# Optimization experiments

Hardware: AMD Instinct MI355X
Metric: run time of the kernel (lower is better)

The kernel has to match this reference:

```python
import jax, jax.numpy as jnp
import numpy as np

B, N, D, H = 8, 2048, 128, 128  # batch, num_nodes, input_size, hidden_size


def setup_inputs() -> dict:
    key = jax.random.key(0)
    ks = jax.random.split(key, 10)
    s = 1.0 / np.sqrt(H)
    u = lambda k, shape: jax.random.uniform(k, shape, jnp.float32, -s, s)
    return {
        "x": jax.random.normal(ks[0], (B, N, D), jnp.float32),
        "adj_matrix": jax.random.randint(ks[1], (B, N, N), 0, 2, jnp.int32),
        # PyTorch LSTM params, gate order (i, f, g, o); forward + backward dirs
        "w_ih_f": u(ks[2], (4 * H, D)),
        "w_hh_f": u(ks[3], (4 * H, H)),
        "b_ih_f": u(ks[4], (4 * H,)),
        "b_hh_f": u(ks[5], (4 * H,)),
        "w_ih_b": u(ks[6], (4 * H, D)),
        "w_hh_b": u(ks[7], (4 * H, H)),
        "b_ih_b": u(ks[8], (4 * H,)),
        "b_hh_b": u(ks[9], (4 * H,)),
    }


def _lstm_last_h(xp, w_hh):
    # xp: [T, B, 4H] precomputed input projection + biases; returns final h [B, H]
    b = xp.shape[1]
    h0 = jnp.zeros((b, H), xp.dtype)
    c0 = jnp.zeros((b, H), xp.dtype)

    def step(carry, xt):
        h, c = carry
        gates = xt + h @ w_hh.T
        i, f, g, o = jnp.split(gates, 4, axis=-1)
        c = jax.nn.sigmoid(f) * c + jax.nn.sigmoid(i) * jnp.tanh(g)
        h = jax.nn.sigmoid(o) * jnp.tanh(c)
        return (h, c), None

    (hT, _), _ = jax.lax.scan(step, (h0, c0), xp)
    return hT


def reference(x, adj_matrix, w_ih_f, w_hh_f, b_ih_f, b_hh_f, w_ih_b, w_hh_b, b_ih_b, b_hh_b):
    x = x.astype(jnp.float32)
    a = (adj_matrix > 0).astype(jnp.float32)  # [B, N, N]
    # mean over {self} + neighbors: (x_i + sum_j a_ij x_j) / (1 + deg_i)
    deg = a.sum(-1, keepdims=True)
    xa = (x + jnp.einsum('bij,bjd->bid', a, x)) / (1.0 + deg)  # [B, N, D]

    seq = jnp.swapaxes(xa, 0, 1)  # [N, B, D], time-major over nodes
    hT_f = _lstm_last_h(seq @ w_ih_f.T + (b_ih_f + b_hh_f), w_hh_f)
    hT_b = _lstm_last_h(seq[::-1] @ w_ih_b.T + (b_ih_b + b_hh_b), w_hh_b)
    return jnp.concatenate([hT_f, hT_b], axis=-1)  # [B, 2H]
```

## Files before the change

### kernel.cpp

```cpp
#include <hip/hip_runtime.h>
#include <math.h>

#define BB 8
#define NN 2048
#define DD 128
#define HH 128

typedef float f4 __attribute__((ext_vector_type(4)));
typedef __attribute__((ext_vector_type(8))) short s16x8;
typedef __attribute__((ext_vector_type(8))) unsigned short u16x8;

__device__ __forceinline__ float fast_rcp(float x) { return __builtin_amdgcn_rcpf(x); }

__device__ __forceinline__ void bsplit(float x, unsigned short& h, unsigned short& l) {
    unsigned u = __float_as_uint(x);
    unsigned r = u + 0x7FFFu + ((u >> 16) & 1u);
    h = (unsigned short)(r >> 16);
    float xh = __uint_as_float(((unsigned)h) << 16);
    float d = x - xh;
    unsigned u2 = __float_as_uint(d);
    unsigned r2 = u2 + 0x7FFFu + ((u2 >> 16) & 1u);
    l = (unsigned short)(r2 >> 16);
}

__global__ __launch_bounds__(256) void k_xT(const float* __restrict__ x,
                                            unsigned short* __restrict__ xth,
                                            unsigned short* __restrict__ xtl) {
    __shared__ __align__(16) unsigned short th[32][72];
    __shared__ __align__(16) unsigned short tl[32][72];
    const int n0 = blockIdx.x * 64;
    const int d0 = blockIdx.y * 32;
    const int b = blockIdx.z;
    const int tid = threadIdx.x;
    {
        const int nl = tid & 63, dseg = tid >> 6;
        const float* xp = x + ((size_t)b * NN + n0 + nl) * DD + d0 + dseg * 8;
        float4 v0 = *(const float4*)(xp);
        float4 v1 = *(const float4*)(xp + 4);
        const float* vv = (const float*)&v0;
#pragma unroll
        for (int j = 0; j < 4; ++j) {
            unsigned short hh, ll;
            bsplit(vv[j], hh, ll);
            th[dseg * 8 + j][nl] = hh;
            tl[dseg * 8 + j][nl] = ll;
        }
        const float* vw = (const float*)&v1;
#pragma unroll
        for (int j = 0; j < 4; ++j) {
            unsigned short hh, ll;
            bsplit(vw[j], hh, ll);
            th[dseg * 8 + 4 + j][nl] = hh;
            tl[dseg * 8 + 4 + j][nl] = ll;
        }
    }
    __syncthreads();
    {
        const int dl = tid >> 3, nseg = tid & 7;
        u16x8 vh = *(const u16x8*)&th[dl][nseg * 8];
        u16x8 vl = *(const u16x8*)&tl[dl][nseg * 8];
        size_t off = ((size_t)b * DD + d0 + dl) * NN + n0 + nseg * 8;
        *(u16x8*)(xth + off) = vh;
        *(u16x8*)(xtl + off) = vl;
    }
}

__global__ __launch_bounds__(256) void k_agg2(const int* __restrict__ adj,
                                              const unsigned short* __restrict__ xth,
                                              const unsigned short* __restrict__ xtl,
                                              float* __restrict__ xa) {
    __shared__ __align__(16) unsigned short Al[64][40];
    __shared__ __align__(16) unsigned short Xh[128][40];
    __shared__ __align__(16) unsigned short Xl[128][40];
    const int b = blockIdx.y;
    const int i0 = blockIdx.x * 64;
    const int tid = threadIdx.x;
    const int wave = tid >> 6, lane = tid & 63;
    const int ar = tid >> 2, aks = (tid & 3) * 8;
    const int xd = tid >> 1, xks = (tid & 1) * 16;
    const int* ap = adj + ((size_t)b * NN + i0 + ar) * NN + aks;
    const unsigned short* hp = xth + ((size_t)b * DD + xd) * NN + xks;
    const unsigned short* lp = xtl + ((size_t)b * DD + xd) * NN + xks;

    f4 acc[8], dacc;
#pragma unroll
    for (int t = 0; t < 8; ++t) acc[t] = {0.f, 0.f, 0.f, 0.f};
    dacc = {0.f, 0.f, 0.f, 0.f};
    const short onebf = (short)0x3F80;
    s16x8 ones = {onebf, onebf, onebf, onebf, onebf, onebf, onebf, onebf};

    int4 a0 = *(const int4*)(ap);
    int4 a1 = *(const int4*)(ap + 4);
    u16x8 h0 = *(const u16x8*)(hp);
    u16x8 h1 = *(const u16x8*)(hp + 8);
    u16x8 l0 = *(const u16x8*)(lp);
    u16x8 l1 = *(const u16x8*)(lp + 8);

    for (int k0 = 0; k0 < NN; k0 += 32) {
        {
            u16x8 w;
            const int* av0 = (const int*)&a0;
            const int* av1 = (const int*)&a1;
            int colb = k0 + aks, myrow = i0 + ar;
#pragma unroll
            for (int j = 0; j < 4; ++j) {
                int c0 = (av0[j] > 0 ? 1 : 0) + (myrow == colb + j ? 1 : 0);
                int c1 = (av1[j] > 0 ? 1 : 0) + (myrow == colb + 4 + j ? 1 : 0);
                w[j] = c0 == 0 ? 0 : (c0 == 1 ? 0x3F80 : 0x4000);
                w[4 + j] = c1 == 0 ? 0 : (c1 == 1 ? 0x3F80 : 0x4000);
            }
            *(u16x8*)&Al[ar][aks] = w;
            *(u16x8*)&Xh[xd][xks] = h0;
            *(u16x8*)&Xh[xd][xks + 8] = h1;
            *(u16x8*)&Xl[xd][xks] = l0;
            *(u16x8*)&Xl[xd][xks + 8] = l1;
        }
        __syncthreads();
        if (k0 + 32 < NN) {
            a0 = *(const int4*)(ap + k0 + 32);
            a1 = *(const int4*)(ap + k0 + 36);
            h0 = *(const u16x8*)(hp + k0 + 32);
            h1 = *(const u16x8*)(hp + k0 + 40);
            l0 = *(const u16x8*)(lp + k0 + 32);
            l1 = *(const u16x8*)(lp + k0 + 40);
        }
        s16x8 afr = *(const s16x8*)&Al[16 * wave + (lane & 15)][(lane >> 4) * 8];
#pragma unroll
        for (int t = 0; t < 8; ++t) {
            s16x8 bh = *(const s16x8*)&Xh[16 * t + (lane & 15)][(lane >> 4) * 8];
            s16x8 bl = *(const s16x8*)&Xl[16 * t + (lane & 15)][(lane >> 4) * 8];
            acc[t] = __builtin_amdgcn_mfma_f32_16x16x32_bf16(afr, bh, acc[t], 0, 0, 0);
            acc[t] = __builtin_amdgcn_mfma_f32_16x16x32_bf16(afr, bl, acc[t], 0, 0, 0);
        }
        dacc = __builtin_amdgcn_mfma_f32_16x16x32_bf16(afr, ones, dacc, 0, 0, 0);
        __syncthreads();
    }
    float inv[4];
#pragma unroll
    for (int r = 0; r < 4; ++r) inv[r] = fast_rcp(dacc[r]);
#pragma unroll
    for (int t = 0; t < 8; ++t)
#pragma unroll
        for (int r = 0; r < 4; ++r) {
            int row = i0 + 16 * wave + (lane >> 4) * 4 + r;
            xa[((size_t)b * NN + row) * DD + 16 * t + (lane & 15)] = acc[t][r] * inv[r];
        }
}

#define MT 64
#define GT 32

__global__ __launch_bounds__(256) void k_proj(const float* __restrict__ xa,
                                              const float* __restrict__ wif,
                                              const float* __restrict__ wib,
                                              const float* __restrict__ bif,
                                              const float* __restrict__ bhf,
                                              const float* __restrict__ bib,
                                              const float* __restrict__ bhb,
                                              float* __restrict__ xpf,
                                              float* __restrict__ xpb) {
    __shared__ __align__(16) float xs[MT][132];
    __shared__ __align__(16) float wl[GT][132];
    const int r0 = blockIdx.x * MT;
    const int g0 = blockIdx.y * GT;
    const int tid = threadIdx.x;
#pragma unroll
    for (int k = 0; k < 8; ++k) {
        int idx = tid + k * 256;
        int row = idx >> 5, c4 = idx & 31;
        int r = r0 + row;
        int t = r >> 3, bb = r & 7;
        float4 v = *(const float4*)(xa + ((size_t)bb * NN + t) * DD + c4 * 4);
        *(float4*)(&xs[row][c4 * 4]) = v;
    }
#pragma unroll
    for (int k = 0; k < 4; ++k) {
        int idx = tid + k * 256;
        int row = idx >> 5, c4 = idx & 31;
        int g = g0 + row;
        const float* wsrc = (g < 512) ? (wif + (size_t)g * DD) : (wib + (size_t)(g - 512) * DD);
        *(float4*)(&wl[row][c4 * 4]) = *(const float4*)(wsrc + c4 * 4);
    }
    __syncthreads();
    const int mg = tid >> 4;
    const int gg = tid & 15;
    float acc[4][2];
#pragma unroll
    for (int i = 0; i < 4; ++i) { acc[i][0] = 0.f; acc[i][1] = 0.f; }
#pragma unroll 8
    for (int d4 = 0; d4 < 32; ++d4) {
        float4 xv[4], wv[2];
#pragma unroll
        for (int i = 0; i < 4; ++i) xv[i] = *(const float4*)(&xs[mg * 4 + i][d4 * 4]);
        wv[0] = *(const float4*)(&wl[gg * 2 + 0][d4 * 4]);
        wv[1] = *(const float4*)(&wl[gg * 2 + 1][d4 * 4]);
#pragma unroll
        for (int i = 0; i < 4; ++i) {
#pragma unroll
            for (int j = 0; j < 2; ++j) {
                acc[i][j] = fmaf(xv[i].x, wv[j].x, acc[i][j]);
                acc[i][j] = fmaf(xv[i].y, wv[j].y, acc[i][j]);
                acc[i][j] = fmaf(xv[i].z, wv[j].z, acc[i][j]);
                acc[i][j] = fmaf(xv[i].w, wv[j].w, acc[i][j]);
            }
        }
    }
#pragma unroll
    for (int j = 0; j < 2; ++j) {
        int g = g0 + gg * 2 + j;
        float bias = (g < 512) ? (bif[g] + bhf[g]) : (bib[g - 512] + bhb[g - 512]);
#pragma unroll
        for (int i = 0; i < 4; ++i) {
            int r = r0 + mg * 4 + i;
            int t = r >> 3, bb = r & 7;
            float v = acc[i][j] + bias;
            if (g < 512) {
                int p = 4 * (g & 127) + (g >> 7);
                xpf[((size_t)t * BB + bb) * 512 + p] = v;
            } else {
                int gb = g - 512;
                int p = 4 * (gb & 127) + (gb >> 7);
                xpb[((size_t)(NN - 1 - t) * BB + bb) * 512 + p] = v;
            }
        }
    }
}


#define STRG(x) #x
#define WLD(R0, R3, WOFF, IMM)                                            \
    "global_load_dwordx4 v[" STRG(R0) ":" STRG(R3) "], %[" STRG(WOFF) "], %[whs] offset:" STRG(IMM) "\n\t"
#define PKQ(H0, H1, A0, A1, B0, B1, C0, C1, D0, D1)                                        \
    "v_pk_fma_f32 v[24:25], v[" STRG(A0) ":" STRG(A1) "], v[" STRG(H0) ":" STRG(H1) "], v[24:25]\n\t" \
    "v_pk_fma_f32 v[26:27], v[" STRG(B0) ":" STRG(B1) "], v[" STRG(H0) ":" STRG(H1) "], v[26:27]\n\t" \
    "v_pk_fma_f32 v[28:29], v[" STRG(C0) ":" STRG(C1) "], v[" STRG(H0) ":" STRG(H1) "], v[28:29]\n\t" \
    "v_pk_fma_f32 v[30:31], v[" STRG(D0) ":" STRG(D1) "], v[" STRG(H0) ":" STRG(H1) "], v[30:31]\n\t"
#define PKQ0(H0, H1, A0, A1, B0, B1, C0, C1, D0, D1)                                       \
    "v_pk_mul_f32 v[24:25], v[" STRG(A0) ":" STRG(A1) "], v[" STRG(H0) ":" STRG(H1) "]\n\t" \
    "v_pk_mul_f32 v[26:27], v[" STRG(B0) ":" STRG(B1) "], v[" STRG(H0) ":" STRG(H1) "]\n\t" \
    "v_pk_mul_f32 v[28:29], v[" STRG(C0) ":" STRG(C1) "], v[" STRG(H0) ":" STRG(H1) "]\n\t" \
    "v_pk_mul_f32 v[30:31], v[" STRG(D0) ":" STRG(D1) "], v[" STRG(H0) ":" STRG(H1) "]\n\t"

__global__ __launch_bounds__(512) void k_lstm(const float* __restrict__ xpf,
                                              const float* __restrict__ xpb,
                                              const float* __restrict__ whf,
                                              const float* __restrict__ whb,
                                              float* __restrict__ out) {
    const int b = blockIdx.x;
    const int dir = blockIdx.y;
    const float* __restrict__ xp = dir ? xpb : xpf;
    const float* __restrict__ wh = dir ? whb : whf;
    const int t = threadIdx.x;
    const int q = t >> 2;
    const int jq = t & 3;

    __shared__ __align__(64) float h_lds[1088];
    for (int i = t; i < 1088; i += 512) h_lds[i] = 0.f;
    __syncthreads();

    unsigned hbase = (unsigned)(uintptr_t)&h_lds[0];
    unsigned rd0 = hbase + 672u * (unsigned)jq;
    unsigned rdd = rd0 ^ (rd0 + 2176u);
    unsigned wr0 = hbase + 2176u + 544u * (unsigned)jq + ((unsigned)q << 2);
    unsigned wrd = wr0 ^ (wr0 - 2176u);
    unsigned w0 = ((0u * 128u + (unsigned)q) * 128u + (unsigned)jq * 32u) * 4u;
    unsigned w1 = ((1u * 128u + (unsigned)q) * 128u + (unsigned)jq * 32u) * 4u;
    unsigned w2 = ((2u * 128u + (unsigned)q) * 128u + (unsigned)jq * 32u) * 4u;
    unsigned w3 = ((3u * 128u + (unsigned)q) * 128u + (unsigned)jq * 32u) * 4u;
    unsigned xoff = (unsigned)(b * 512 + t) * 4u + 16384u;
    float xp0v = xp[(size_t)b * 512 + t];
    float s0 = (jq == 0) ? 1.f : 0.f;
    float s1 = (jq == 1) ? 1.f : 0.f;
    float s2 = (jq == 2) ? 1.f : 0.f;
    float s3 = (jq == 3) ? 1.f : 0.f;
    float mlv = (jq == 2) ? -2.8853900817779268f : -1.4426950408889634f;
    float Aav = (jq == 2) ? 2.f : 1.f;
    float Bav = (jq == 2) ? -1.f : 0.f;
    float h_out;

    asm volatile(
        "v_mov_b32 v16, 0\n\t"
        "s_movk_i32 s20, 0x800\n\t"
        "v_mov_b32 v19, %[x0]\n\t"
        "v_mov_b32 v21, %[xo]\n\t"
        "v_mov_b32 v22, %[rdb]\n\t"
        "v_mov_b32 v23, %[wrb]\n\t"
        WLD(64, 67, w0, 0) WLD(68, 71, w0, 16) WLD(72, 75, w0, 32) WLD(76, 79, w0, 48)
        WLD(80, 83, w0, 64) WLD(84, 87, w0, 80) WLD(88, 91, w0, 96) WLD(92, 95, w0, 112)
        WLD(96, 99, w1, 0) WLD(100, 103, w1, 16) WLD(104, 107, w1, 32) WLD(108, 111, w1, 48)
        WLD(112, 115, w1, 64) WLD(116, 119, w1, 80) WLD(120, 123, w1, 96) WLD(124, 127, w1, 112)
        WLD(128, 131, w2, 0) WLD(132, 135, w2, 16) WLD(136, 139, w2, 32) WLD(140, 143, w2, 48)
        WLD(144, 147, w2, 64) WLD(148, 151, w2, 80) WLD(152, 155, w2, 96) WLD(156, 159, w2, 112)
        WLD(160, 163, w3, 0) WLD(164, 167, w3, 16) WLD(168, 171, w3, 32) WLD(172, 175, w3, 48)
        WLD(176, 179, w3, 64) WLD(180, 183, w3, 80) WLD(184, 187, w3, 96) WLD(188, 191, w3, 112)
        "s_waitcnt vmcnt(0)\n\t"
        "LSTM_TOP%=:\n\t"
        "global_load_dword v20, v21, %[xps]\n\t"
        "ds_read_b128 v[32:35], v22\n\t"
        "ds_read_b128 v[36:39], v22 offset:16\n\t"
        "ds_read_b128 v[40:43], v22 offset:32\n\t"
        "ds_read_b128 v[44:47], v22 offset:48\n\t"
        "ds_read_b128 v[48:51], v22 offset:64\n\t"
        "ds_read_b128 v[52:55], v22 offset:80\n\t"
        "ds_read_b128 v[56:59], v22 offset:96\n\t"
        "ds_read_b128 v[60:63], v22 offset:112\n\t"
        "v_xor_b32 v22, %[rdd], v22\n\t"
        "v_add_u32 v21, 0x4000, v21\n\t"
        "s_waitcnt lgkmcnt(7)\n\t"
        PKQ0(32, 33, 64, 65, 96, 97, 128, 129, 160, 161)
        PKQ(34, 35, 66, 67, 98, 99, 130, 131, 162, 163)
        "s_waitcnt lgkmcnt(6)\n\t"
        PKQ(36, 37, 68, 69, 100, 101, 132, 133, 164, 165)
        PKQ(38, 39, 70, 71, 102, 103, 134, 135, 166, 167)
        "s_waitcnt lgkmcnt(5)\n\t"
        PKQ(40, 41, 72, 73, 104, 105, 136, 137, 168, 169)
        PKQ(42, 43, 74, 75, 106, 107, 138, 139, 170, 171)
        "s_waitcnt lgkmcnt(4)\n\t"
        PKQ(44, 45, 76, 77, 108, 109, 140, 141, 172, 173)
        PKQ(46, 47, 78, 79, 110, 111, 142, 143, 174, 175)
        "s_waitcnt lgkmcnt(3)\n\t"
        PKQ(48, 49, 80, 81, 112, 113, 144, 145, 176, 177)
        PKQ(50, 51, 82, 83, 114, 115, 146, 147, 178, 179)
        "s_waitcnt lgkmcnt(2)\n\t"
        PKQ(52, 53, 84, 85, 116, 117, 148, 149, 180, 181)
        PKQ(54, 55, 86, 87, 118, 119, 150, 151, 182, 183)
        "s_waitcnt lgkmcnt(1)\n\t"
        PKQ(56, 57, 88, 89, 120, 121, 152, 153, 184, 185)
        PKQ(58, 59, 90, 91, 122, 123, 154, 155, 186, 187)
        "s_waitcnt lgkmcnt(0)\n\t"
        PKQ(60, 61, 92, 93, 124, 125, 156, 157, 188, 189)
        PKQ(62, 63, 94, 95, 126, 127, 158, 159, 190, 191)
        "v_add_f32 v8, v24, v25\n\t"
        "v_add_f32 v9, v26, v27\n\t"
        "v_add_f32 v10, v28, v29\n\t"
        "v_add_f32 v11, v30, v31\n\t"
        "v_mov_b32_dpp v12, v8 quad_perm:[1,0,3,2] row_mask:0xf bank_mask:0xf\n\t"
        "v_mov_b32_dpp v13, v9 quad_perm:[1,0,3,2] row_mask:0xf bank_mask:0xf\n\t"
        "v_mov_b32_dpp v14, v10 quad_perm:[1,0,3,2] row_mask:0xf bank_mask:0xf\n\t"
        "v_mov_b32_dpp v15, v11 quad_perm:[1,0,3,2] row_mask:0xf bank_mask:0xf\n\t"
        "v_add_f32 v8, v8, v12\n\t"
        "v_add_f32 v9, v9, v13\n\t"
        "v_add_f32 v10, v10, v14\n\t"
        "v_add_f32 v11, v11, v15\n\t"
        "v_mov_b32_dpp v12, v8 quad_perm:[2,3,0,1] row_mask:0xf bank_mask:0xf\n\t"
        "v_mov_b32_dpp v13, v9 quad_perm:[2,3,0,1] row_mask:0xf bank_mask:0xf\n\t"
        "v_mov_b32_dpp v14, v10 quad_perm:[2,3,0,1] row_mask:0xf bank_mask:0xf\n\t"
        "v_mov_b32_dpp v15, v11 quad_perm:[2,3,0,1] row_mask:0xf bank_mask:0xf\n\t"
        "v_add_f32 v8, v8, v12\n\t"
        "v_add_f32 v9, v9, v13\n\t"
        "v_add_f32 v10, v10, v14\n\t"
        "v_add_f32 v11, v11, v15\n\t"
        "v_mul_f32 v12, %[s0], v8\n\t"
        "v_fma_f32 v12, %[s1], v9, v12\n\t"
        "v_fma_f32 v12, %[s2], v10, v12\n\t"
        "v_fma_f32 v12, %[s3], v11, v12\n\t"
        "v_add_f32 v12, v12, v19\n\t"
        "v_mul_f32 v13, %[ml], v12\n\t"
        "v_exp_f32 v13, v13\n\t"
        "s_nop 1\n\t"
        "v_add_f32 v13, 1.0, v13\n\t"
        "v_rcp_f32 v13, v13\n\t"
        "s_nop 1\n\t"
        "v_fma_f32 v12, %[Aa], v13, %[Ba]\n\t"
        "s_nop 1\n\t"
        "v_mov_b32_dpp v13, v12 quad_perm:[0,0,0,0] row_mask:0xf bank_mask:0xf\n\t"
        "v_mov_b32_dpp v14, v12 quad_perm:[2,2,2,2] row_mask:0xf bank_mask:0xf\n\t"
        "v_mov_b32_dpp v15, v12 quad_perm:[1,1,1,1] row_mask:0xf bank_mask:0xf\n\t"
        "v_mov_b32_dpp v17, v12 quad_perm:[3,3,3,3] row_mask:0xf bank_mask:0xf\n\t"
        "v_mul_f32 v13, v13, v14\n\t"
        "v_fma_f32 v16, v15, v16, v13\n\t"
        "v_mul_f32 v14, 0xc038aa3b, v16\n\t"
        "v_exp_f32 v14, v14\n\t"
        "s_nop 1\n\t"
        "v_add_f32 v14, 1.0, v14\n\t"
        "v_rcp_f32 v14, v14\n\t"
        "s_nop 1\n\t"
        "v_fma_f32 v14, 2.0, v14, -1.0\n\t"
        "v_mul_f32 v17, v14, v17\n\t"
        "ds_write_b32 v23, v17\n\t"
        "s_waitcnt lgkmcnt(0)\n\t"
        "s_barrier\n\t"
        "s_waitcnt vmcnt(0)\n\t"
        "v_mov_b32 v19, v20\n\t"
        "v_xor_b32 v23, %[wrd], v23\n\t"
        "s_sub_u32 s20, s20, 1\n\t"
        "s_cmp_lg_u32 s20, 0\n\t"
        "s_cbranch_scc1 LSTM_TOP%=\n\t"
        "v_mov_b32 %[ho], v17\n\t"
        : [ho] "=v"(h_out)
        : [w0] "v"(w0), [w1] "v"(w1), [w2] "v"(w2), [w3] "v"(w3),
          [whs] "s"(wh), [xps] "s"(xp),
          [xo] "v"(xoff), [rdb] "v"(rd0), [wrb] "v"(wr0),
          [rdd] "v"(rdd), [wrd] "v"(wrd), [x0] "v"(xp0v),
          [s0] "v"(s0), [s1] "v"(s1), [s2] "v"(s2), [s3] "v"(s3),
          [ml] "v"(mlv), [Aa] "v"(Aav), [Ba] "v"(Bav)
        : "memory", "vcc", "scc", "s20",
          "v8", "v9", "v10", "v11", "v12", "v13", "v14", "v15", "v16", "v17",
          "v18", "v19", "v20", "v21", "v22", "v23", "v24", "v25", "v26", "v27",
          "v28", "v29", "v30", "v31", "v32", "v33", "v34", "v35", "v36", "v37",
          "v38", "v39", "v40", "v41", "v42", "v43", "v44", "v45", "v46", "v47",
          "v48", "v49", "v50", "v51", "v52", "v53", "v54", "v55", "v56", "v57",
          "v58", "v59", "v60", "v61", "v62", "v63", "v64", "v65", "v66", "v67",
          "v68", "v69", "v70", "v71", "v72", "v73", "v74", "v75", "v76", "v77",
          "v78", "v79", "v80", "v81", "v82", "v83", "v84", "v85", "v86", "v87",
          "v88", "v89", "v90", "v91", "v92", "v93", "v94", "v95", "v96", "v97",
          "v98", "v99", "v100", "v101", "v102", "v103", "v104", "v105", "v106", "v107",
          "v108", "v109", "v110", "v111", "v112", "v113", "v114", "v115", "v116", "v117",
          "v118", "v119", "v120", "v121", "v122", "v123", "v124", "v125", "v126", "v127",
          "v128", "v129", "v130", "v131", "v132", "v133", "v134", "v135", "v136", "v137",
          "v138", "v139", "v140", "v141", "v142", "v143", "v144", "v145", "v146", "v147",
          "v148", "v149", "v150", "v151", "v152", "v153", "v154", "v155", "v156", "v157",
          "v158", "v159", "v160", "v161", "v162", "v163", "v164", "v165", "v166", "v167",
          "v168", "v169", "v170", "v171", "v172", "v173", "v174", "v175", "v176", "v177",
          "v178", "v179", "v180", "v181", "v182", "v183", "v184", "v185", "v186", "v187",
          "v188", "v189", "v190", "v191");

    if (jq == 0) out[(size_t)b * 256 + dir * HH + q] = h_out;
}

extern "C" void kernel_launch(void* const* d_in, const int* in_sizes, int n_in,
                              void* d_out, int out_size, void* d_ws, size_t ws_size,
                              hipStream_t stream) {
    const float* x = (const float*)d_in[0];
    const int* adj = (const int*)d_in[1];
    const float* wif = (const float*)d_in[2];
    const float* whf = (const float*)d_in[3];
    const float* bif = (const float*)d_in[4];
    const float* bhf = (const float*)d_in[5];
    const float* wib = (const float*)d_in[6];
    const float* whb = (const float*)d_in[7];
    const float* bib = (const float*)d_in[8];
    const float* bhb = (const float*)d_in[9];
    float* out = (float*)d_out;

    float* xpf = (float*)d_ws;
    float* xpb = xpf + (size_t)NN * BB * 512;
    float* xa = xpb + (size_t)NN * BB * 512;
    unsigned short* xth = (unsigned short*)xpf;
    unsigned short* xtl = xth + (size_t)BB * DD * NN;

    k_xT<<<dim3(NN / 64, DD / 32, BB), 256, 0, stream>>>(x, xth, xtl);
    k_agg2<<<dim3(NN / 64, BB), 256, 0, stream>>>(adj, xth, xtl, xa);
    k_proj<<<dim3((NN * BB) / MT, 1024 / GT), 256, 0, stream>>>(xa, wif, wib, bif, bhf, bib, bhb,
                                                                xpf, xpb);
    k_lstm<<<dim3(BB, 2), 512, 0, stream>>>(xpf, xpb, whf, whb, out);
}
```

Before: 1.247 ms.

## Move input projection to split-bf16 MFMA and unroll LSTM loop by two

The aggregation kernel now writes its output as hi/lo bf16 pairs. A new projection kernel then computes the LSTM input projection with three bf16 MFMAs per tile (hi*hi, lo*hi, hi*lo) instead of scalar fp32 FMAs, converting the weights to bf16 pairs in shared memory. The LSTM recurrence loop is unrolled by two with separate ping-pong LDS addresses and xp registers, which removes the per-step xor and register moves. The split-bf16 scheme drops the lo*lo term, so precision is slightly reduced. Each projection block also redoes the weight conversion.

New measurement: 1.209 ms. 3.0% less time.

```diff
diff --git a/kernel.cpp b/kernel.cpp
--- a/kernel.cpp
+++ b/kernel.cpp
@@ -68,7 +68,8 @@
 __global__ __launch_bounds__(256) void k_agg2(const int* __restrict__ adj,
                                               const unsigned short* __restrict__ xth,
                                               const unsigned short* __restrict__ xtl,
-                                              float* __restrict__ xa) {
+                                              unsigned short* __restrict__ xah,
+                                              unsigned short* __restrict__ xal) {
     __shared__ __align__(16) unsigned short Al[64][40];
     __shared__ __align__(16) unsigned short Xh[128][40];
     __shared__ __align__(16) unsigned short Xl[128][40];
@@ -143,84 +144,82 @@
 #pragma unroll
         for (int r = 0; r < 4; ++r) {
             int row = i0 + 16 * wave + (lane >> 4) * 4 + r;
-            xa[((size_t)b * NN + row) * DD + 16 * t + (lane & 15)] = acc[t][r] * inv[r];
-        }
-}
-
-#define MT 64
-#define GT 32
-
-__global__ __launch_bounds__(256) void k_proj(const float* __restrict__ xa,
-                                              const float* __restrict__ wif,
-                                              const float* __restrict__ wib,
-                                              const float* __restrict__ bif,
-                                              const float* __restrict__ bhf,
-                                              const float* __restrict__ bib,
-                                              const float* __restrict__ bhb,
-                                              float* __restrict__ xpf,
-                                              float* __restrict__ xpb) {
-    __shared__ __align__(16) float xs[MT][132];
-    __shared__ __align__(16) float wl[GT][132];
-    const int r0 = blockIdx.x * MT;
-    const int g0 = blockIdx.y * GT;
+            float v = acc[t][r] * inv[r];
+            unsigned short hh, ll;
+            bsplit(v, hh, ll);
+            size_t base = ((size_t)b * NN + row) * DD + 16 * t + (lane & 15);
+            xah[base] = hh;
+            xal[base] = ll;
+        }
+}
+
+__global__ __launch_bounds__(256) void k_proj2(const unsigned short* __restrict__ xah,
+                                               const unsigned short* __restrict__ xal,
+                                               const float* __restrict__ wif,
+                                               const float* __restrict__ wib,
+                                               const float* __restrict__ bif,
+                                               const float* __restrict__ bhf,
+                                               const float* __restrict__ bib,
+                                               const float* __restrict__ bhb,
+                                               float* __restrict__ xpf,
+                                               float* __restrict__ xpb) {
+    __shared__ __align__(16) unsigned short Wh[128][132];
+    __shared__ __align__(16) unsigned short Wl[128][132];
+    const int rr0 = blockIdx.x * 64;
+    const int n0 = blockIdx.y * 128;
     const int tid = threadIdx.x;
-#pragma unroll
-    for (int k = 0; k < 8; ++k) {
-        int idx = tid + k * 256;
-        int row = idx >> 5, c4 = idx & 31;
-        int r = r0 + row;
-        int t = r >> 3, bb = r & 7;
-        float4 v = *(const float4*)(xa + ((size_t)bb * NN + t) * DD + c4 * 4);
-        *(float4*)(&xs[row][c4 * 4]) = v;
-    }
-#pragma unroll
-    for (int k = 0; k < 4; ++k) {
-        int idx = tid + k * 256;
-        int row = idx >> 5, c4 = idx & 31;
-        int g = g0 + row;
-        const float* wsrc = (g < 512) ? (wif + (size_t)g * DD) : (wib + (size_t)(g - 512) * DD);
-        *(float4*)(&wl[row][c4 * 4]) = *(const float4*)(wsrc + c4 * 4);
+    const int wave = tid >> 6, lane = tid & 63;
+    {
+        int g = tid >> 1;
+        int d0 = (tid & 1) * 64;
+        int gg = n0 + g;
+        const float* wsrc = (gg < 512) ? (wif + (size_t)gg * DD) : (wib + (size_t)(gg - 512) * DD);
+#pragma unroll
+        for (int j = 0; j < 64; j += 4) {
+            float4 v = *(const float4*)(wsrc + d0 + j);
+            unsigned short hh, ll;
+            bsplit(v.x, hh, ll); Wh[g][d0 + j + 0] = hh; Wl[g][d0 + j + 0] = ll;
+            bsplit(v.y, hh, ll); Wh[g][d0 + j + 1] = hh; Wl[g][d0 + j + 1] = ll;
+            bsplit(v.z, hh, ll); Wh[g][d0 + j + 2] = hh; Wl[g][d0 + j + 2] = ll;
+            bsplit(v.w, hh, ll); Wh[g][d0 + j + 3] = hh; Wl[g][d0 + j + 3] = ll;
+        }
     }
     __syncthreads();
-    const int mg = tid >> 4;
-    const int gg = tid & 15;
-    float acc[4][2];
-#pragma unroll
-    for (int i = 0; i < 4; ++i) { acc[i][0] = 0.f; acc[i][1] = 0.f; }
-#pragma unroll 8
-    for (int d4 = 0; d4 < 32; ++d4) {
-        float4 xv[4], wv[2];
-#pragma unroll
-        for (int i = 0; i < 4; ++i) xv[i] = *(const float4*)(&xs[mg * 4 + i][d4 * 4]);
-        wv[0] = *(const float4*)(&wl[gg * 2 + 0][d4 * 4]);
-        wv[1] = *(const float4*)(&wl[gg * 2 + 1][d4 * 4]);
-#pragma unroll
-        for (int i = 0; i < 4; ++i) {
-#pragma unroll
-            for (int j = 0; j < 2; ++j) {
-                acc[i][j] = fmaf(xv[i].x, wv[j].x, acc[i][j]);
-                acc[i][j] = fmaf(xv[i].y, wv[j].y, acc[i][j]);
-                acc[i][j] = fmaf(xv[i].z, wv[j].z, acc[i][j]);
-                acc[i][j] = fmaf(xv[i].w, wv[j].w, acc[i][j]);
-            }
-        }
-    }
-#pragma unroll
-    for (int j = 0; j < 2; ++j) {
-        int g = g0 + gg * 2 + j;
-        float bias = (g < 512) ? (bif[g] + bhf[g]) : (bib[g - 512] + bhb[g - 512]);
-#pragma unroll
-        for (int i = 0; i < 4; ++i) {
-            int r = r0 + mg * 4 + i;
-            int t = r >> 3, bb = r & 7;
-            float v = acc[i][j] + bias;
-            if (g < 512) {
-                int p = 4 * (g & 127) + (g >> 7);
-                xpf[((size_t)t * BB + bb) * 512 + p] = v;
+    const int arow = rr0 + wave * 16 + (lane & 15);
+    const unsigned short* ah = xah + (size_t)arow * DD + ((lane >> 4) * 8);
+    const unsigned short* al = xal + (size_t)arow * DD + ((lane >> 4) * 8);
+    f4 acc[8];
+#pragma unroll
+    for (int nt = 0; nt < 8; ++nt) acc[nt] = {0.f, 0.f, 0.f, 0.f};
+#pragma unroll
+    for (int k0 = 0; k0 < DD; k0 += 32) {
+        s16x8 afh = *(const s16x8*)(ah + k0);
+        s16x8 afl = *(const s16x8*)(al + k0);
+#pragma unroll
+        for (int nt = 0; nt < 8; ++nt) {
+            s16x8 bh = *(const s16x8*)&Wh[nt * 16 + (lane & 15)][k0 + (lane >> 4) * 8];
+            s16x8 bl = *(const s16x8*)&Wl[nt * 16 + (lane & 15)][k0 + (lane >> 4) * 8];
+            acc[nt] = __builtin_amdgcn_mfma_f32_16x16x32_bf16(afh, bh, acc[nt], 0, 0, 0);
+            acc[nt] = __builtin_amdgcn_mfma_f32_16x16x32_bf16(afl, bh, acc[nt], 0, 0, 0);
+            acc[nt] = __builtin_amdgcn_mfma_f32_16x16x32_bf16(afh, bl, acc[nt], 0, 0, 0);
+        }
+    }
+#pragma unroll
+    for (int nt = 0; nt < 8; ++nt) {
+        int gg = n0 + nt * 16 + (lane & 15);
+        float bias = (gg < 512) ? (bif[gg] + bhf[gg]) : (bib[gg - 512] + bhb[gg - 512]);
+#pragma unroll
+        for (int r = 0; r < 4; ++r) {
+            int rr = rr0 + wave * 16 + (lane >> 4) * 4 + r;
+            int b = rr >> 11, t = rr & 2047;
+            float v = acc[nt][r] + bias;
+            if (gg < 512) {
+                int pp = 4 * (gg & 127) + (gg >> 7);
+                xpf[((size_t)t * BB + b) * 512 + pp] = v;
             } else {
-                int gb = g - 512;
-                int p = 4 * (gb & 127) + (gb >> 7);
-                xpb[((size_t)(NN - 1 - t) * BB + bb) * 512 + p] = v;
+                int gb = gg - 512;
+                int pp = 4 * (gb & 127) + (gb >> 7);
+                xpb[((size_t)(NN - 1 - t) * BB + b) * 512 + pp] = v;
             }
         }
     }
@@ -241,6 +240,93 @@
     "v_pk_mul_f32 v[28:29], v[" STRG(C0) ":" STRG(C1) "], v[" STRG(H0) ":" STRG(H1) "]\n\t" \
     "v_pk_mul_f32 v[30:31], v[" STRG(D0) ":" STRG(D1) "], v[" STRG(H0) ":" STRG(H1) "]\n\t"
 
+#define LSTM_BODY(XPD, XPU, RD, WR)                                                        \
+    "global_load_dword " XPD ", v21, %[xps]\n\t"                                           \
+    "ds_read_b128 v[32:35], " RD "\n\t"                                                    \
+    "ds_read_b128 v[36:39], " RD " offset:16\n\t"                                          \
+    "ds_read_b128 v[40:43], " RD " offset:32\n\t"                                          \
+    "ds_read_b128 v[44:47], " RD " offset:48\n\t"                                          \
+    "ds_read_b128 v[48:51], " RD " offset:64\n\t"                                          \
+    "ds_read_b128 v[52:55], " RD " offset:80\n\t"                                          \
+    "ds_read_b128 v[56:59], " RD " offset:96\n\t"                                          \
+    "ds_read_b128 v[60:63], " RD " offset:112\n\t"                                         \
+    "v_add_u32 v21, 0x4000, v21\n\t"                                                       \
+    "s_waitcnt lgkmcnt(7)\n\t"                                                             \
+    PKQ0(32, 33, 64, 65, 96, 97, 128, 129, 160, 161)                                       \
+    PKQ(34, 35, 66, 67, 98, 99, 130, 131, 162, 163)                                        \
+    "s_waitcnt lgkmcnt(6)\n\t"                                                             \
+    PKQ(36, 37, 68, 69, 100, 101, 132, 133, 164, 165)                                      \
+    PKQ(38, 39, 70, 71, 102, 103, 134, 135, 166, 167)                                      \
+    "s_waitcnt lgkmcnt(5)\n\t"                                                             \
+    PKQ(40, 41, 72, 73, 104, 105, 136, 137, 168, 169)                                      \
+    PKQ(42, 43, 74, 75, 106, 107, 138, 139, 170, 171)                                      \
+    "s_waitcnt lgkmcnt(4)\n\t"                                                             \
+    PKQ(44, 45, 76, 77, 108, 109, 140, 141, 172, 173)                                      \
+    PKQ(46, 47, 78, 79, 110, 111, 142, 143, 174, 175)                                      \
+    "s_waitcnt lgkmcnt(3)\n\t"                                                             \
+    PKQ(48, 49, 80, 81, 112, 113, 144, 145, 176, 177)                                      \
+    PKQ(50, 51, 82, 83, 114, 115, 146, 147, 178, 179)                                      \
+    "s_waitcnt lgkmcnt(2)\n\t"                                                             \
+    PKQ(52, 53, 84, 85, 116, 117, 148, 149, 180, 181)                                      \
+    PKQ(54, 55, 86, 87, 118, 119, 150, 151, 182, 183)                                      \
+    "s_waitcnt lgkmcnt(1)\n\t"                                                             \
+    PKQ(56, 57, 88, 89, 120, 121, 152, 153, 184, 185)                                      \
+    PKQ(58, 59, 90, 91, 122, 123, 154, 155, 186, 187)                                      \
+    "s_waitcnt lgkmcnt(0)\n\t"                                                             \
+    PKQ(60, 61, 92, 93, 124, 125, 156, 157, 188, 189)                                      \
+    PKQ(62, 63, 94, 95, 126, 127, 158, 159, 190, 191)                                      \
+    "v_add_f32 v8, v24, v25\n\t"                                                           \
+    "v_add_f32 v9, v26, v27\n\t"                                                           \
+    "v_add_f32 v10, v28, v29\n\t"                                                          \
+    "v_add_f32 v11, v30, v31\n\t"                                                          \
+    "v_mov_b32_dpp v12, v8 quad_perm:[1,0,3,2] row_mask:0xf bank_mask:0xf\n\t"             \
+    "v_mov_b32_dpp v13, v9 quad_perm:[1,0,3,2] row_mask:0xf bank_mask:0xf\n\t"             \
+    "v_mov_b32_dpp v14, v10 quad_perm:[1,0,3,2] row_mask:0xf bank_mask:0xf\n\t"            \
+    "v_mov_b32_dpp v15, v11 quad_perm:[1,0,3,2] row_mask:0xf bank_mask:0xf\n\t"            \
+    "v_add_f32 v8, v8, v12\n\t"                                                            \
+    "v_add_f32 v9, v9, v13\n\t"                                                            \
+    "v_add_f32 v10, v10, v14\n\t"                                                          \
+    "v_add_f32 v11, v11, v15\n\t"                                                          \
+    "v_mov_b32_dpp v12, v8 quad_perm:[2,3,0,1] row_mask:0xf bank_mask:0xf\n\t"             \
+    "v_mov_b32_dpp v13, v9 quad_perm:[2,3,0,1] row_mask:0xf bank_mask:0xf\n\t"             \
+    "v_mov_b32_dpp v14, v10 quad_perm:[2,3,0,1] row_mask:0xf bank_mask:0xf\n\t"            \
+    "v_mov_b32_dpp v15, v11 quad_perm:[2,3,0,1] row_mask:0xf bank_mask:0xf\n\t"            \
+    "v_add_f32 v8, v8, v12\n\t"                                                            \
+    "v_add_f32 v9, v9, v13\n\t"                                                            \
+    "v_add_f32 v10, v10, v14\n\t"                                                          \
+    "v_add_f32 v11, v11, v15\n\t"                                                          \
+    "v_mul_f32 v12, %[s0], v8\n\t"                                                         \
+    "v_fma_f32 v12, %[s1], v9, v12\n\t"                                                    \
+    "v_fma_f32 v12, %[s2], v10, v12\n\t"                                                   \
+    "s_waitcnt vmcnt(1)\n\t"                                                               \
+    "v_fma_f32 v12, %[s3], v11, v12\n\t"                                                   \
+    "v_add_f32 v12, v12, " XPU "\n\t"                                                      \
+    "v_mul_f32 v13, %[ml], v12\n\t"                                                        \
+    "v_exp_f32 v13, v13\n\t"                                                               \
+    "s_nop 1\n\t"                                                                          \
+    "v_add_f32 v13, 1.0, v13\n\t"                                                          \
+    "v_rcp_f32 v13, v13\n\t"                                                               \
+    "s_nop 1\n\t"                                                                          \
+    "v_fma_f32 v12, %[Aa], v13, %[Ba]\n\t"                                                 \
+    "s_nop 1\n\t"                                                                          \
+    "v_mov_b32_dpp v13, v12 quad_perm:[0,0,0,0] row_mask:0xf bank_mask:0xf\n\t"            \
+    "v_mov_b32_dpp v14, v12 quad_perm:[2,2,2,2] row_mask:0xf bank_mask:0xf\n\t"            \
+    "v_mov_b32_dpp v15, v12 quad_perm:[1,1,1,1] row_mask:0xf bank_mask:0xf\n\t"            \
+    "v_mov_b32_dpp v17, v12 quad_perm:[3,3,3,3] row_mask:0xf bank_mask:0xf\n\t"            \
+    "v_mul_f32 v13, v13, v14\n\t"                                                          \
+    "v_fma_f32 v16, v15, v16, v13\n\t"                                                     \
+    "v_mul_f32 v14, 0xc038aa3b, v16\n\t"                                                   \
+    "v_exp_f32 v14, v14\n\t"                                                               \
+    "s_nop 1\n\t"                                                                          \
+    "v_add_f32 v14, 1.0, v14\n\t"                                                          \
+    "v_rcp_f32 v14, v14\n\t"                                                               \
+    "s_nop 1\n\t"                                                                          \
+    "v_fma_f32 v14, 2.0, v14, -1.0\n\t"                                                    \
+    "v_mul_f32 v17, v14, v17\n\t"                                                          \
+    "ds_write_b32 " WR ", v17\n\t"                                                         \
+    "s_waitcnt lgkmcnt(0)\n\t"                                                             \
+    "s_barrier\n\t"
+
 __global__ __launch_bounds__(512) void k_lstm(const float* __restrict__ xpf,
                                               const float* __restrict__ xpb,
                                               const float* __restrict__ whf,
@@ -260,9 +346,9 @@
 
     unsigned hbase = (unsigned)(uintptr_t)&h_lds[0];
     unsigned rd0 = hbase + 672u * (unsigned)jq;
-    unsigned rdd = rd0 ^ (rd0 + 2176u);
-    unsigned wr0 = hbase + 2176u + 544u * (unsigned)jq + ((unsigned)q << 2);
-    unsigned wrd = wr0 ^ (wr0 - 2176u);
+    unsigned rd1 = rd0 + 2176u;
+    unsigned wrE = hbase + 2176u + 544u * (unsigned)jq + ((unsigned)q << 2);
+    unsigned wrO = wrE - 2176u;
     unsigned w0 = ((0u * 128u + (unsigned)q) * 128u + (unsigned)jq * 32u) * 4u;
     unsigned w1 = ((1u * 128u + (unsigned)q) * 128u + (unsigned)jq * 32u) * 4u;
     unsigned w2 = ((2u * 128u + (unsigned)q) * 128u + (unsigned)jq * 32u) * 4u;
@@ -280,11 +366,13 @@
 
     asm volatile(
         "v_mov_b32 v16, 0\n\t"
-        "s_movk_i32 s20, 0x800\n\t"
+        "s_movk_i32 s20, 0x400\n\t"
         "v_mov_b32 v19, %[x0]\n\t"
         "v_mov_b32 v21, %[xo]\n\t"
         "v_mov_b32 v22, %[rdb]\n\t"
+        "v_mov_b32 v18, %[rdb2]\n\t"
         "v_mov_b32 v23, %[wrb]\n\t"
+        "v_mov_b32 v192, %[wrb2]\n\t"
         WLD(64, 67, w0, 0) WLD(68, 71, w0, 16) WLD(72, 75, w0, 32) WLD(76, 79, w0, 48)
         WLD(80, 83, w0, 64) WLD(84, 87, w0, 80) WLD(88, 91, w0, 96) WLD(92, 95, w0, 112)
         WLD(96, 99, w1, 0) WLD(100, 103, w1, 16) WLD(104, 107, w1, 32) WLD(108, 111, w1, 48)
@@ -295,94 +383,8 @@
         WLD(176, 179, w3, 64) WLD(180, 183, w3, 80) WLD(184, 187, w3, 96) WLD(188, 191, w3, 112)
         "s_waitcnt vmcnt(0)\n\t"
         "LSTM_TOP%=:\n\t"
-        "global_load_dword v20, v21, %[xps]\n\t"
-        "ds_read_b128 v[32:35], v22\n\t"
-        "ds_read_b128 v[36:39], v22 offset:16\n\t"
-        "ds_read_b128 v[40:43], v22 offset:32\n\t"
-        "ds_read_b128 v[44:47], v22 offset:48\n\t"
-        "ds_read_b128 v[48:51], v22 offset:64\n\t"
-        "ds_read_b128 v[52:55], v22 offset:80\n\t"
-        "ds_read_b128 v[56:59], v22 offset:96\n\t"
-        "ds_read_b128 v[60:63], v22 offset:112\n\t"
-        "v_xor_b32 v22, %[rdd], v22\n\t"
-        "v_add_u32 v21, 0x4000, v21\n\t"
-        "s_waitcnt lgkmcnt(7)\n\t"
-        PKQ0(32, 33, 64, 65, 96, 97, 128, 129, 160, 161)
-        PKQ(34, 35, 66, 67, 98, 99, 130, 131, 162, 163)
-        "s_waitcnt lgkmcnt(6)\n\t"
-        PKQ(36, 37, 68, 69, 100, 101, 132, 133, 164, 165)
-        PKQ(38, 39, 70, 71, 102, 103, 134, 135, 166, 167)
-        "s_waitcnt lgkmcnt(5)\n\t"
-        PKQ(40, 41, 72, 73, 104, 105, 136, 137, 168, 169)
-        PKQ(42, 43, 74, 75, 106, 107, 138, 139, 170, 171)
-        "s_waitcnt lgkmcnt(4)\n\t"
-        PKQ(44, 45, 76, 77, 108, 109, 140, 141, 172, 173)
-        PKQ(46, 47, 78, 79, 110, 111, 142, 143, 174, 175)
-        "s_waitcnt lgkmcnt(3)\n\t"
-        PKQ(48, 49, 80, 81, 112, 113, 144, 145, 176, 177)
-        PKQ(50, 51, 82, 83, 114, 115, 146, 147, 178, 179)
-        "s_waitcnt lgkmcnt(2)\n\t"
-        PKQ(52, 53, 84, 85, 116, 117, 148, 149, 180, 181)
-        PKQ(54, 55, 86, 87, 118, 119, 150, 151, 182, 183)
-        "s_waitcnt lgkmcnt(1)\n\t"
-        PKQ(56, 57, 88, 89, 120, 121, 152, 153, 184, 185)
-        PKQ(58, 59, 90, 91, 122, 123, 154, 155, 186, 187)
-        "s_waitcnt lgkmcnt(0)\n\t"
-        PKQ(60, 61, 92, 93, 124, 125, 156, 157, 188, 189)
-        PKQ(62, 63, 94, 95, 126, 127, 158, 159, 190, 191)
-        "v_add_f32 v8, v24, v25\n\t"
-        "v_add_f32 v9, v26, v27\n\t"
-        "v_add_f32 v10, v28, v29\n\t"
-        "v_add_f32 v11, v30, v31\n\t"
-        "v_mov_b32_dpp v12, v8 quad_perm:[1,0,3,2] row_mask:0xf bank_mask:0xf\n\t"
-        "v_mov_b32_dpp v13, v9 quad_perm:[1,0,3,2] row_mask:0xf bank_mask:0xf\n\t"
-        "v_mov_b32_dpp v14, v10 quad_perm:[1,0,3,2] row_mask:0xf bank_mask:0xf\n\t"
-        "v_mov_b32_dpp v15, v11 quad_perm:[1,0,3,2] row_mask:0xf bank_mask:0xf\n\t"
-        "v_add_f32 v8, v8, v12\n\t"
-        "v_add_f32 v9, v9, v13\n\t"
-        "v_add_f32 v10, v10, v14\n\t"
-        "v_add_f32 v11, v11, v15\n\t"
-        "v_mov_b32_dpp v12, v8 quad_perm:[2,3,0,1] row_mask:0xf bank_mask:0xf\n\t"
-        "v_mov_b32_dpp v13, v9 quad_perm:[2,3,0,1] row_mask:0xf bank_mask:0xf\n\t"
-        "v_mov_b32_dpp v14, v10 quad_perm:[2,3,0,1] row_mask:0xf bank_mask:0xf\n\t"
-        "v_mov_b32_dpp v15, v11 quad_perm:[2,3,0,1] row_mask:0xf bank_mask:0xf\n\t"
-        "v_add_f32 v8, v8, v12\n\t"
-        "v_add_f32 v9, v9, v13\n\t"
-        "v_add_f32 v10, v10, v14\n\t"
-        "v_add_f32 v11, v11, v15\n\t"
-        "v_mul_f32 v12, %[s0], v8\n\t"
-        "v_fma_f32 v12, %[s1], v9, v12\n\t"
-        "v_fma_f32 v12, %[s2], v10, v12\n\t"
-        "v_fma_f32 v12, %[s3], v11, v12\n\t"
-        "v_add_f32 v12, v12, v19\n\t"
-        "v_mul_f32 v13, %[ml], v12\n\t"
-        "v_exp_f32 v13, v13\n\t"
-        "s_nop 1\n\t"
-        "v_add_f32 v13, 1.0, v13\n\t"
-        "v_rcp_f32 v13, v13\n\t"
-        "s_nop 1\n\t"
-        "v_fma_f32 v12, %[Aa], v13, %[Ba]\n\t"
-        "s_nop 1\n\t"
-        "v_mov_b32_dpp v13, v12 quad_perm:[0,0,0,0] row_mask:0xf bank_mask:0xf\n\t"
-        "v_mov_b32_dpp v14, v12 quad_perm:[2,2,2,2] row_mask:0xf bank_mask:0xf\n\t"
-        "v_mov_b32_dpp v15, v12 quad_perm:[1,1,1,1] row_mask:0xf bank_mask:0xf\n\t"
-        "v_mov_b32_dpp v17, v12 quad_perm:[3,3,3,3] row_mask:0xf bank_mask:0xf\n\t"
-        "v_mul_f32 v13, v13, v14\n\t"
-        "v_fma_f32 v16, v15, v16, v13\n\t"
-        "v_mul_f32 v14, 0xc038aa3b, v16\n\t"
-        "v_exp_f32 v14, v14\n\t"
-        "s_nop 1\n\t"
-        "v_add_f32 v14, 1.0, v14\n\t"
-        "v_rcp_f32 v14, v14\n\t"
-        "s_nop 1\n\t"
-        "v_fma_f32 v14, 2.0, v14, -1.0\n\t"
-        "v_mul_f32 v17, v14, v17\n\t"
-        "ds_write_b32 v23, v17\n\t"
-        "s_waitcnt lgkmcnt(0)\n\t"
-        "s_barrier\n\t"
-        "s_waitcnt vmcnt(0)\n\t"
-        "v_mov_b32 v19, v20\n\t"
-        "v_xor_b32 v23, %[wrd], v23\n\t"
+        LSTM_BODY("v20", "v19", "v22", "v23")
+        LSTM_BODY("v19", "v20", "v18", "v192")
         "s_sub_u32 s20, s20, 1\n\t"
         "s_cmp_lg_u32 s20, 0\n\t"
         "s_cbranch_scc1 LSTM_TOP%=\n\t"
@@ -390,8 +392,8 @@
         : [ho] "=v"(h_out)
         : [w0] "v"(w0), [w1] "v"(w1), [w2] "v"(w2), [w3] "v"(w3),
           [whs] "s"(wh), [xps] "s"(xp),
-          [xo] "v"(xoff), [rdb] "v"(rd0), [wrb] "v"(wr0),
-          [rdd] "v"(rdd), [wrd] "v"(wrd), [x0] "v"(xp0v),
+          [xo] "v"(xoff), [rdb] "v"(rd0), [rdb2] "v"(rd1),
+          [wrb] "v"(wrE), [wrb2] "v"(wrO), [x0] "v"(xp0v),
           [s0] "v"(s0), [s1] "v"(s1), [s2] "v"(s2), [s3] "v"(s3),
           [ml] "v"(mlv), [Aa] "v"(Aav), [Ba] "v"(Bav)
         : "memory", "vcc", "scc", "s20",
@@ -413,7 +415,7 @@
           "v158", "v159", "v160", "v161", "v162", "v163", "v164", "v165", "v166", "v167",
           "v168", "v169", "v170", "v171", "v172", "v173", "v174", "v175", "v176", "v177",
           "v178", "v179", "v180", "v181", "v182", "v183", "v184", "v185", "v186", "v187",
-          "v188", "v189", "v190", "v191");
+          "v188", "v189", "v190", "v191", "v192");
 
     if (jq == 0) out[(size_t)b * 256 + dir * HH + q] = h_out;
 }
@@ -435,13 +437,14 @@
 
     float* xpf = (float*)d_ws;
     float* xpb = xpf + (size_t)NN * BB * 512;
-    float* xa = xpb + (size_t)NN * BB * 512;
+    unsigned short* xah = (unsigned short*)(xpb + (size_t)NN * BB * 512);
+    unsigned short* xal = xah + (size_t)BB * NN * DD;
     unsigned short* xth = (unsigned short*)xpf;
     unsigned short* xtl = xth + (size_t)BB * DD * NN;
 
     k_xT<<<dim3(NN / 64, DD / 32, BB), 256, 0, stream>>>(x, xth, xtl);
-    k_agg2<<<dim3(NN / 64, BB), 256, 0, stream>>>(adj, xth, xtl, xa);
-    k_proj<<<dim3((NN * BB) / MT, 1024 / GT), 256, 0, stream>>>(xa, wif, wib, bif, bhf, bib, bhb,
-                                                                xpf, xpb);
+    k_agg2<<<dim3(NN / 64, BB), 256, 0, stream>>>(adj, xth, xtl, xah, xal);
+    k_proj2<<<dim3((NN * BB) / 64, 1024 / 128), 256, 0, stream>>>(xah, xal, wif, wib, bif, bhf,
+                                                                  bib, bhb, xpf, xpb);
     k_lstm<<<dim3(BB, 2), 512, 0, stream>>>(xpf, xpb, whf, whb, out);
 }
```
